# Kernel tuning notes

Hardware: AMD Instinct MI355X
Metric: run time of the kernel (lower is better)

The kernel has to match this reference:

```python
import jax, jax.numpy as jnp
import numpy as np

N = 100000
E = 1600000
IN_DIM, HID, OUT = 128, 64, 32
SLOPE = 0.1


def setup_inputs() -> dict:
    key = jax.random.key(0)
    ks = jax.random.split(key, 8)
    x = jax.random.normal(ks[0], (N, IN_DIM), dtype=jnp.float32)
    edge_index = jax.random.randint(ks[1], (2, E), 0, N, dtype=jnp.int64)
    s1 = 1.0 / np.sqrt(IN_DIM)
    s2 = 1.0 / np.sqrt(HID)
    W_l1 = jax.random.uniform(ks[2], (IN_DIM, HID), jnp.float32, -s1, s1)
    W_r1 = jax.random.uniform(ks[3], (IN_DIM, HID), jnp.float32, -s1, s1)
    b1 = jax.random.uniform(ks[4], (HID,), jnp.float32, -s1, s1)
    W_l2 = jax.random.uniform(ks[5], (HID, OUT), jnp.float32, -s2, s2)
    W_r2 = jax.random.uniform(ks[6], (HID, OUT), jnp.float32, -s2, s2)
    b2 = jax.random.uniform(ks[7], (OUT,), jnp.float32, -s2, s2)
    return {"x": x, "edge_index": edge_index,
            "W_l1": W_l1, "W_r1": W_r1, "b1": b1,
            "W_l2": W_l2, "W_r2": W_r2, "b2": b2}


def _sage_conv(h, src, dst, deg_inv, W_l, W_r, b):
    # mean-aggregate neighbor features: gather from src, scatter-add to dst
    agg = jax.ops.segment_sum(h[src], dst, num_segments=N) * deg_inv  # [N, d]
    return agg @ W_l + h @ W_r + b


def reference(x, edge_index, W_l1, W_r1, b1, W_l2, W_r2, b2):
    src, dst = edge_index[0], edge_index[1]
    deg = jax.ops.segment_sum(jnp.ones((E,), x.dtype), dst, num_segments=N)
    deg_inv = (1.0 / jnp.maximum(deg, 1.0))[:, None]  # [N, 1]
    h = jax.nn.leaky_relu(_sage_conv(x, src, dst, deg_inv, W_l1, W_r1, b1), SLOPE)
    z = jax.nn.leaky_relu(_sage_conv(h, src, dst, deg_inv, W_l2, W_r2, b2), SLOPE)
    return z
```

## Files before the change

### kernel.cpp

```cpp
#include <hip/hip_runtime.h>


constexpr int IN_DIM  = 128;
constexpr int HID     = 64;
constexpr int OUT_DIM = 32;
constexpr float SLOPE = 0.1f;
constexpr int NPB_SHIFT = 8;
constexpr int NBMAX = 512;
constexpr int CHUNK = 4096;

typedef unsigned int uint32;
typedef unsigned short ushort16;

__device__ inline float blo(uint32 u) { return __uint_as_float(u << 16); }
__device__ inline float bhi(uint32 u) { return __uint_as_float(u & 0xffff0000u); }
__device__ inline ushort16 f2b(float f) {
    uint32 u = __float_as_uint(f);
    u += 0x7fffu + ((u >> 16) & 1u);
    return (ushort16)(u >> 16);
}
__device__ inline uint32 pack2(float lo, float hi) {
    return (uint32)f2b(lo) | ((uint32)f2b(hi) << 16);
}

__global__ __launch_bounds__(256) void bucket_hist_kernel(
    const int* __restrict__ dst, int* __restrict__ bhist, int E) {
    __shared__ int bh[NBMAX];
    for (int i = threadIdx.x; i < NBMAX; i += 256) bh[i] = 0;
    __syncthreads();
    for (int e = blockIdx.x * 256 + threadIdx.x; e < E; e += gridDim.x * 256)
        atomicAdd(&bh[dst[e] >> NPB_SHIFT], 1);
    __syncthreads();
    for (int b = threadIdx.x; b < NBMAX; b += 256)
        if (bh[b]) atomicAdd(&bhist[b], bh[b]);
}

__global__ __launch_bounds__(512) void bucket_scan_kernel(
    const int* __restrict__ bhist, int* __restrict__ ebase,
    int* __restrict__ pbase, int* __restrict__ bcur,
    int* __restrict__ rowptr, int NB, int N, int E) {
    __shared__ int s1[512], s2[512];
    const int t = threadIdx.x;
    int bh = (t < NB) ? bhist[t] : 0;
    int pd = (bh + 15) & ~15;
    s1[t] = bh; s2[t] = pd; __syncthreads();
    for (int off = 1; off < 512; off <<= 1) {
        int a = (t >= off) ? s1[t - off] : 0;
        int b = (t >= off) ? s2[t - off] : 0;
        __syncthreads();
        s1[t] += a; s2[t] += b;
        __syncthreads();
    }
    ebase[t] = s1[t] - bh;
    pbase[t] = s2[t] - pd;
    bcur[t]  = s2[t] - pd;
    if (t == 0) rowptr[N] = E;
}

__global__ __launch_bounds__(256) void partition_kernel(
    const int* __restrict__ src, const int* __restrict__ dst,
    int* __restrict__ bcur, uint32* __restrict__ pairs, int E, int NB) {
    __shared__ int hist[NBMAX], loff[NBMAX], cur[NBMAX];
    __shared__ int s[256];
    __shared__ uint32 stage[CHUNK];
    const int tid = threadIdx.x;
    const int e0  = blockIdx.x * CHUNK;
    const int cnt = min(CHUNK, E - e0);
    for (int i = tid; i < NBMAX; i += 256) hist[i] = 0;
    __syncthreads();
    int sreg[16], dreg[16];
#pragma unroll
    for (int k = 0; k < 16; ++k) {
        int i = tid + k * 256;
        if (i < cnt) {
            sreg[k] = src[e0 + i];
            dreg[k] = dst[e0 + i];
            atomicAdd(&hist[dreg[k] >> NPB_SHIFT], 1);
        }
    }
    __syncthreads();
    int a0 = hist[2 * tid], a1 = hist[2 * tid + 1];
    s[tid] = a0 + a1; __syncthreads();
    for (int off = 1; off < 256; off <<= 1) {
        int t = (tid >= off) ? s[tid - off] : 0;
        __syncthreads();
        s[tid] += t;
        __syncthreads();
    }
    int ex = s[tid] - (a0 + a1);
    loff[2 * tid] = ex;      loff[2 * tid + 1] = ex + a0;
    cur[2 * tid]  = ex;      cur[2 * tid + 1]  = ex + a0;
    __syncthreads();
#pragma unroll
    for (int k = 0; k < 16; ++k) {
        int i = tid + k * 256;
        if (i < cnt) {
            int b = dreg[k] >> NPB_SHIFT;
            int pos = atomicAdd(&cur[b], 1);
            stage[pos] = (uint32)sreg[k] | ((uint32)(dreg[k] & 255) << 24);
        }
    }
    __syncthreads();
    for (int b = tid; b < NB; b += 256) {
        int cb = hist[b];
        if (cb) {
            int g  = atomicAdd(&bcur[b], cb);
            int lb = loff[b];
            for (int k = 0; k < cb; ++k) pairs[g + k] = stage[lb + k];
        }
    }
}

__global__ __launch_bounds__(256) void fine_bin_kernel(
    const uint32* __restrict__ pairs, const int* __restrict__ bhist,
    const int* __restrict__ ebase, const int* __restrict__ pbase,
    int* __restrict__ rowptr, int* __restrict__ srcs, int N) {
    __shared__ int h2[256], cur[256], s[256];
    const int tid  = threadIdx.x;
    const int b    = blockIdx.x;
    const int n0   = b << NPB_SHIFT;
    const int base = pbase[b];
    const int sz   = bhist[b];
    h2[tid] = 0;
    __syncthreads();
    for (int i = tid; i < sz; i += 256)
        atomicAdd(&h2[pairs[base + i] >> 24], 1);
    __syncthreads();
    int v = h2[tid]; s[tid] = v; __syncthreads();
    for (int off = 1; off < 256; off <<= 1) {
        int t = (tid >= off) ? s[tid - off] : 0;
        __syncthreads();
        s[tid] += t;
        __syncthreads();
    }
    int rp = ebase[b] + s[tid] - v;
    int n  = n0 + tid;
    if (n < N) rowptr[n] = rp;
    cur[tid] = rp;
    __syncthreads();
    for (int i = tid; i < sz; i += 256) {
        uint32 u = pairs[base + i];
        int p = atomicAdd(&cur[u >> 24], 1);
        srcs[p] = (int)(u & 0xFFFFFFu);
    }
}

__global__ __launch_bounds__(256) void gemm1_mfma_kernel(
    const float* __restrict__ x, const float* __restrict__ Wl,
    const float* __restrict__ Wr, const float* __restrict__ b1,
    ushort16* __restrict__ xl, float* __restrict__ xr, int N) {
    using frag = __attribute__((ext_vector_type(8))) short;
    using f32x4 = __attribute__((ext_vector_type(4))) float;
    constexpr int LDA = IN_DIM + 8;
    __shared__ ushort16 Ash[64][LDA];
    __shared__ ushort16 Bsh[128][LDA];
    const int tid = threadIdx.x;
    const int n0  = blockIdx.x * 64;
    {
        const int c = tid & 63;
        for (int k = tid >> 6; k < IN_DIM; k += 4) {
            Bsh[c][k]      = f2b(Wl[k * HID + c]);
            Bsh[c + 64][k] = f2b(Wr[k * HID + c]);
        }
    }
    {
        const int lc  = (tid & 31) * 4;
        for (int row = tid >> 5; row < 64; row += 8) {
            int node = n0 + row;
            float4 xv = (node < N)
                ? *reinterpret_cast<const float4*>(&x[(long)node * IN_DIM + lc])
                : float4{0.f, 0.f, 0.f, 0.f};
            ushort16 pk[4] = {f2b(xv.x), f2b(xv.y), f2b(xv.z), f2b(xv.w)};
            *reinterpret_cast<ushort2*>(&Ash[row][lc])     = ushort2{pk[0], pk[1]};
            *reinterpret_cast<ushort2*>(&Ash[row][lc + 2]) = ushort2{pk[2], pk[3]};
        }
    }
    __syncthreads();
    const int lane = tid & 63;
    const int m0   = (tid >> 6) * 16;
    const int mlo  = lane & 15;
    const int qk   = lane >> 4;
    frag Af[4];
#pragma unroll
    for (int kc = 0; kc < 4; ++kc)
        Af[kc] = *reinterpret_cast<const frag*>(&Ash[m0 + mlo][kc * 32 + qk * 8]);
#pragma unroll
    for (int ct = 0; ct < 8; ++ct) {
        f32x4 acc = {0.f, 0.f, 0.f, 0.f};
#pragma unroll
        for (int kc = 0; kc < 4; ++kc) {
            frag Bf = *reinterpret_cast<const frag*>(&Bsh[ct * 16 + mlo][kc * 32 + qk * 8]);
            acc = __builtin_amdgcn_mfma_f32_16x16x32_bf16(Af[kc], Bf, acc, 0, 0, 0);
        }
        const int col = ct * 16 + mlo;
#pragma unroll
        for (int r = 0; r < 4; ++r) {
            int node = n0 + m0 + qk * 4 + r;
            if (node < N) {
                if (col < HID) xl[(long)node * HID + col] = f2b(acc[r]);
                else           xr[(long)node * HID + (col - HID)] = acc[r] + b1[col - HID];
            }
        }
    }
}

__global__ __launch_bounds__(256) void agg_mid_kernel(
    const int* __restrict__ rowptr, const int* __restrict__ srcs,
    const uint4* __restrict__ xlq,
    const float* __restrict__ xr,
    const float* __restrict__ Wl2, const float* __restrict__ Wr2,
    const float* __restrict__ b2,
    uint4* __restrict__ hlq,
    float* __restrict__ hr, int N) {
    __shared__ float Wc[HID][HID];
    for (int i = threadIdx.x; i < HID * HID; i += 256) {
        int k = i >> 6, c = i & 63;
        Wc[k][c] = (c < OUT_DIM) ? Wl2[k * OUT_DIM + c]
                                 : Wr2[k * OUT_DIM + (c - OUT_DIM)];
    }
    __syncthreads();
    const int lane  = threadIdx.x & 63;
    const int li    = lane & 7;
    const int gbase = lane & 56;
    const int wave  = (blockIdx.x << 2) + (threadIdx.x >> 6);
    const int n     = wave * 8 + (lane >> 3);
    if (n >= N) return;
    const int rp = rowptr[n];
    const int d  = rowptr[n + 1] - rp;
    float acc[8] = {};
    int j = 0;
    while (j + 8 <= d) {
        int sidb = srcs[rp + j + li];
#pragma unroll
        for (int t = 0; t < 8; ++t) {
            int s = __shfl(sidb, gbase + t);
            uint4 u = xlq[(long)s * 8 + li];
            acc[0] += blo(u.x); acc[1] += bhi(u.x);
            acc[2] += blo(u.y); acc[3] += bhi(u.y);
            acc[4] += blo(u.z); acc[5] += bhi(u.z);
            acc[6] += blo(u.w); acc[7] += bhi(u.w);
        }
        j += 8;
    }
    int r = d - j;
    if (r > 0) {
        int sidb = srcs[rp + j + ((li < r) ? li : 0)];
#pragma unroll
        for (int t = 0; t < 7; ++t) {
            if (t < r) {
                int s = __shfl(sidb, gbase + t);
                uint4 u = xlq[(long)s * 8 + li];
                acc[0] += blo(u.x); acc[1] += bhi(u.x);
                acc[2] += blo(u.y); acc[3] += bhi(u.y);
                acc[4] += blo(u.z); acc[5] += bhi(u.z);
                acc[6] += blo(u.w); acc[7] += bhi(u.w);
            }
        }
    }
    const float dinv = (d > 0) ? (1.f / (float)d) : 1.f;
    float4 xrA = *reinterpret_cast<const float4*>(&xr[(long)n * HID + 8 * li]);
    float4 xrB = *reinterpret_cast<const float4*>(&xr[(long)n * HID + 8 * li + 4]);
    float h[8];
    h[0] = fmaf(acc[0], dinv, xrA.x); h[1] = fmaf(acc[1], dinv, xrA.y);
    h[2] = fmaf(acc[2], dinv, xrA.z); h[3] = fmaf(acc[3], dinv, xrA.w);
    h[4] = fmaf(acc[4], dinv, xrB.x); h[5] = fmaf(acc[5], dinv, xrB.y);
    h[6] = fmaf(acc[6], dinv, xrB.z); h[7] = fmaf(acc[7], dinv, xrB.w);
#pragma unroll
    for (int t = 0; t < 8; ++t) h[t] = (h[t] > 0.f) ? h[t] : SLOPE * h[t];
    float o[8] = {};
#pragma unroll
    for (int k = 0; k < HID; ++k) {
        float hk = __shfl(h[k & 7], gbase + (k >> 3));
        float4 wA = *reinterpret_cast<const float4*>(&Wc[k][8 * li]);
        float4 wB = *reinterpret_cast<const float4*>(&Wc[k][8 * li + 4]);
        o[0] = fmaf(hk, wA.x, o[0]); o[1] = fmaf(hk, wA.y, o[1]);
        o[2] = fmaf(hk, wA.z, o[2]); o[3] = fmaf(hk, wA.w, o[3]);
        o[4] = fmaf(hk, wB.x, o[4]); o[5] = fmaf(hk, wB.y, o[5]);
        o[6] = fmaf(hk, wB.z, o[6]); o[7] = fmaf(hk, wB.w, o[7]);
    }
    if (li < 4) {
        uint4 pk;
        pk.x = pack2(o[0], o[1]); pk.y = pack2(o[2], o[3]);
        pk.z = pack2(o[4], o[5]); pk.w = pack2(o[6], o[7]);
        hlq[(long)n * 4 + li] = pk;
    } else {
        int c0 = 8 * li - 32;
        float4 bA = *reinterpret_cast<const float4*>(&b2[c0]);
        float4 bB = *reinterpret_cast<const float4*>(&b2[c0 + 4]);
        float4 vA = {o[0] + bA.x, o[1] + bA.y, o[2] + bA.z, o[3] + bA.w};
        float4 vB = {o[4] + bB.x, o[5] + bB.y, o[6] + bB.z, o[7] + bB.w};
        *reinterpret_cast<float4*>(&hr[(long)n * OUT_DIM + c0]) = vA;
        *reinterpret_cast<float4*>(&hr[(long)n * OUT_DIM + c0 + 4]) = vB;
    }
}

__global__ __launch_bounds__(256) void agg2_final_kernel(
    const int* __restrict__ rowptr, const int* __restrict__ srcs,
    const uint4* __restrict__ hlq,
    const float* __restrict__ hr,
    float* __restrict__ z, int N) {
    const int lane  = threadIdx.x & 63;
    const int li    = lane & 3;
    const int gbase = lane & 60;
    const int wave  = (blockIdx.x << 2) + (threadIdx.x >> 6);
    const int n     = wave * 16 + (lane >> 2);
    if (n >= N) return;
    const int rp = rowptr[n];
    const int d  = rowptr[n + 1] - rp;
    float acc[8] = {};
    int j = 0;
    while (j + 8 <= d) {
        int sA = srcs[rp + j + li];
        int sB = srcs[rp + j + 4 + li];
#pragma unroll
        for (int t = 0; t < 4; ++t) {
            int s0 = __shfl(sA, gbase + t);
            int s1 = __shfl(sB, gbase + t);
            uint4 u0 = hlq[(long)s0 * 4 + li];
            uint4 u1 = hlq[(long)s1 * 4 + li];
            acc[0] += blo(u0.x); acc[1] += bhi(u0.x);
            acc[2] += blo(u0.y); acc[3] += bhi(u0.y);
            acc[4] += blo(u0.z); acc[5] += bhi(u0.z);
            acc[6] += blo(u0.w); acc[7] += bhi(u0.w);
            acc[0] += blo(u1.x); acc[1] += bhi(u1.x);
            acc[2] += blo(u1.y); acc[3] += bhi(u1.y);
            acc[4] += blo(u1.z); acc[5] += bhi(u1.z);
            acc[6] += blo(u1.w); acc[7] += bhi(u1.w);
        }
        j += 8;
    }
    int r = d - j;
    if (r > 0) {
        int sA = srcs[rp + j + ((li < r) ? li : 0)];
        int sB = srcs[rp + j + ((4 + li < r) ? 4 + li : 0)];
#pragma unroll
        for (int t = 0; t < 4; ++t) {
            if (t < r) {
                int s = __shfl(sA, gbase + t);
                uint4 u = hlq[(long)s * 4 + li];
                acc[0] += blo(u.x); acc[1] += bhi(u.x);
                acc[2] += blo(u.y); acc[3] += bhi(u.y);
                acc[4] += blo(u.z); acc[5] += bhi(u.z);
                acc[6] += blo(u.w); acc[7] += bhi(u.w);
            }
            if (t + 4 < r) {
                int s = __shfl(sB, gbase + t);
                uint4 u = hlq[(long)s * 4 + li];
                acc[0] += blo(u.x); acc[1] += bhi(u.x);
                acc[2] += blo(u.y); acc[3] += bhi(u.y);
                acc[4] += blo(u.z); acc[5] += bhi(u.z);
                acc[6] += blo(u.w); acc[7] += bhi(u.w);
            }
        }
    }
    const float dinv = (d > 0) ? (1.f / (float)d) : 1.f;
    float4 hA = *reinterpret_cast<const float4*>(&hr[(long)n * OUT_DIM + 8 * li]);
    float4 hB = *reinterpret_cast<const float4*>(&hr[(long)n * OUT_DIM + 8 * li + 4]);
    float4 vA, vB;
    vA.x = fmaf(acc[0], dinv, hA.x); vA.y = fmaf(acc[1], dinv, hA.y);
    vA.z = fmaf(acc[2], dinv, hA.z); vA.w = fmaf(acc[3], dinv, hA.w);
    vB.x = fmaf(acc[4], dinv, hB.x); vB.y = fmaf(acc[5], dinv, hB.y);
    vB.z = fmaf(acc[6], dinv, hB.z); vB.w = fmaf(acc[7], dinv, hB.w);
    vA.x = (vA.x > 0.f) ? vA.x : SLOPE * vA.x;
    vA.y = (vA.y > 0.f) ? vA.y : SLOPE * vA.y;
    vA.z = (vA.z > 0.f) ? vA.z : SLOPE * vA.z;
    vA.w = (vA.w > 0.f) ? vA.w : SLOPE * vA.w;
    vB.x = (vB.x > 0.f) ? vB.x : SLOPE * vB.x;
    vB.y = (vB.y > 0.f) ? vB.y : SLOPE * vB.y;
    vB.z = (vB.z > 0.f) ? vB.z : SLOPE * vB.z;
    vB.w = (vB.w > 0.f) ? vB.w : SLOPE * vB.w;
    *reinterpret_cast<float4*>(&z[(long)n * OUT_DIM + 8 * li]) = vA;
    *reinterpret_cast<float4*>(&z[(long)n * OUT_DIM + 8 * li + 4]) = vB;
}

extern "C" void kernel_launch(void* const* d_in, const int* in_sizes, int n_in,
                              void* d_out, int out_size, void* d_ws, size_t ws_size,
                              hipStream_t stream) {
    const float* x   = (const float*)d_in[0];
    const int*   ei  = (const int*)d_in[1];
    const float* Wl1 = (const float*)d_in[2];
    const float* Wr1 = (const float*)d_in[3];
    const float* b1  = (const float*)d_in[4];
    const float* Wl2 = (const float*)d_in[5];
    const float* Wr2 = (const float*)d_in[6];
    const float* b2  = (const float*)d_in[7];

    const int N = in_sizes[0] / IN_DIM;
    const int E = in_sizes[1] / 2;
    const int* src = ei;
    const int* dst = ei + E;
    const int NB = (N + 255) >> NPB_SHIFT;

    char* p = (char*)d_ws;
    int* bhist    = (int*)p;           p += sizeof(int) * NBMAX;
    int* ebase    = (int*)p;           p += sizeof(int) * NBMAX;
    int* pbase    = (int*)p;           p += sizeof(int) * NBMAX;
    int* bcur     = (int*)p;           p += sizeof(int) * NBMAX;
    int* rowptr   = (int*)p;           p += sizeof(int) * (N + 4);
    uint32* pairs = (uint32*)p;        p += sizeof(uint32) * ((size_t)E + 16 * NBMAX);
    int* srcs     = (int*)p;           p += sizeof(int) * E;
    ushort16* xl  = (ushort16*)p;      p += sizeof(ushort16) * (size_t)N * HID;
    float* xr     = (float*)p;         p += sizeof(float) * (size_t)N * HID;
    ushort16* hl  = (ushort16*)p;      p += sizeof(ushort16) * (size_t)N * OUT_DIM;
    float* hr     = (float*)p;         p += sizeof(float) * (size_t)N * OUT_DIM;

    hipMemsetAsync(bhist, 0, sizeof(int) * NBMAX, stream);

    bucket_hist_kernel<<<512, 256, 0, stream>>>(dst, bhist, E);
    bucket_scan_kernel<<<1, 512, 0, stream>>>(bhist, ebase, pbase, bcur, rowptr, NB, N, E);
    partition_kernel<<<(E + CHUNK - 1) / CHUNK, 256, 0, stream>>>(src, dst, bcur, pairs, E, NB);
    fine_bin_kernel<<<NB, 256, 0, stream>>>(pairs, bhist, ebase, pbase, rowptr, srcs, N);
    gemm1_mfma_kernel<<<(N + 63) / 64, 256, 0, stream>>>(x, Wl1, Wr1, b1, xl, xr, N);
    agg_mid_kernel<<<(N + 31) / 32, 256, 0, stream>>>(rowptr, srcs, (const uint4*)xl, xr,
                                                      Wl2, Wr2, b2, (uint4*)hl, hr, N);
    agg2_final_kernel<<<(N + 63) / 64, 256, 0, stream>>>(rowptr, srcs, (const uint4*)hl, hr,
                                                         (float*)d_out, N);
}
```

Before: 279.0 us.

## Split layer-2 GEMM into MFMA kernel and batch gather loads in aggregation kernels

The fused aggregation+FMA-GEMM kernel is split into an aggregation kernel that writes h as bf16 and a separate MFMA bf16 GEMM kernel for the layer-2 weights. Both aggregation loops now issue 16 independent gather loads before accumulating, to raise memory-level parallelism. This adds an extra N×64 bf16 round trip and a kernel launch, uses bf16 weights for layer 2, and raises register pressure from the batched loads.

```diff
diff --git a/kernel.cpp b/kernel.cpp
--- a/kernel.cpp
+++ b/kernel.cpp
@@ -21,6 +21,12 @@
 }
 __device__ inline uint32 pack2(float lo, float hi) {
     return (uint32)f2b(lo) | ((uint32)f2b(hi) << 16);
+}
+__device__ inline void addup(float* acc, uint4 u) {
+    acc[0] += blo(u.x); acc[1] += bhi(u.x);
+    acc[2] += blo(u.y); acc[3] += bhi(u.y);
+    acc[4] += blo(u.z); acc[5] += bhi(u.z);
+    acc[6] += blo(u.w); acc[7] += bhi(u.w);
 }
 
 __global__ __launch_bounds__(256) void bucket_hist_kernel(
@@ -204,21 +210,11 @@
     }
 }
 
-__global__ __launch_bounds__(256) void agg_mid_kernel(
+__global__ __launch_bounds__(256) void agg1_kernel(
     const int* __restrict__ rowptr, const int* __restrict__ srcs,
     const uint4* __restrict__ xlq,
     const float* __restrict__ xr,
-    const float* __restrict__ Wl2, const float* __restrict__ Wr2,
-    const float* __restrict__ b2,
-    uint4* __restrict__ hlq,
-    float* __restrict__ hr, int N) {
-    __shared__ float Wc[HID][HID];
-    for (int i = threadIdx.x; i < HID * HID; i += 256) {
-        int k = i >> 6, c = i & 63;
-        Wc[k][c] = (c < OUT_DIM) ? Wl2[k * OUT_DIM + c]
-                                 : Wr2[k * OUT_DIM + (c - OUT_DIM)];
-    }
-    __syncthreads();
+    uint4* __restrict__ hq, int N) {
     const int lane  = threadIdx.x & 63;
     const int li    = lane & 7;
     const int gbase = lane & 56;
@@ -229,31 +225,45 @@
     const int d  = rowptr[n + 1] - rp;
     float acc[8] = {};
     int j = 0;
-    while (j + 8 <= d) {
-        int sidb = srcs[rp + j + li];
+    while (j + 16 <= d) {
+        int sA = srcs[rp + j + li];
+        int sB = srcs[rp + j + 8 + li];
+        uint4 u0[8], u1[8];
 #pragma unroll
         for (int t = 0; t < 8; ++t) {
-            int s = __shfl(sidb, gbase + t);
-            uint4 u = xlq[(long)s * 8 + li];
-            acc[0] += blo(u.x); acc[1] += bhi(u.x);
-            acc[2] += blo(u.y); acc[3] += bhi(u.y);
-            acc[4] += blo(u.z); acc[5] += bhi(u.z);
-            acc[6] += blo(u.w); acc[7] += bhi(u.w);
-        }
+            int s = __shfl(sA, gbase + t);
+            u0[t] = xlq[(long)s * 8 + li];
+        }
+#pragma unroll
+        for (int t = 0; t < 8; ++t) {
+            int s = __shfl(sB, gbase + t);
+            u1[t] = xlq[(long)s * 8 + li];
+        }
+#pragma unroll
+        for (int t = 0; t < 8; ++t) { addup(acc, u0[t]); addup(acc, u1[t]); }
+        j += 16;
+    }
+    if (j + 8 <= d) {
+        int sA = srcs[rp + j + li];
+        uint4 u0[8];
+#pragma unroll
+        for (int t = 0; t < 8; ++t) {
+            int s = __shfl(sA, gbase + t);
+            u0[t] = xlq[(long)s * 8 + li];
+        }
+#pragma unroll
+        for (int t = 0; t < 8; ++t) addup(acc, u0[t]);
         j += 8;
     }
     int r = d - j;
     if (r > 0) {
-        int sidb = srcs[rp + j + ((li < r) ? li : 0)];
+        int sA = srcs[rp + j + ((li < r) ? li : 0)];
 #pragma unroll
         for (int t = 0; t < 7; ++t) {
             if (t < r) {
-                int s = __shfl(sidb, gbase + t);
+                int s = __shfl(sA, gbase + t);
                 uint4 u = xlq[(long)s * 8 + li];
-                acc[0] += blo(u.x); acc[1] += bhi(u.x);
-                acc[2] += blo(u.y); acc[3] += bhi(u.y);
-                acc[4] += blo(u.z); acc[5] += bhi(u.z);
-                acc[6] += blo(u.w); acc[7] += bhi(u.w);
+                addup(acc, u);
             }
         }
     }
@@ -267,30 +277,57 @@
     h[6] = fmaf(acc[6], dinv, xrB.z); h[7] = fmaf(acc[7], dinv, xrB.w);
 #pragma unroll
     for (int t = 0; t < 8; ++t) h[t] = (h[t] > 0.f) ? h[t] : SLOPE * h[t];
-    float o[8] = {};
-#pragma unroll
-    for (int k = 0; k < HID; ++k) {
-        float hk = __shfl(h[k & 7], gbase + (k >> 3));
-        float4 wA = *reinterpret_cast<const float4*>(&Wc[k][8 * li]);
-        float4 wB = *reinterpret_cast<const float4*>(&Wc[k][8 * li + 4]);
-        o[0] = fmaf(hk, wA.x, o[0]); o[1] = fmaf(hk, wA.y, o[1]);
-        o[2] = fmaf(hk, wA.z, o[2]); o[3] = fmaf(hk, wA.w, o[3]);
-        o[4] = fmaf(hk, wB.x, o[4]); o[5] = fmaf(hk, wB.y, o[5]);
-        o[6] = fmaf(hk, wB.z, o[6]); o[7] = fmaf(hk, wB.w, o[7]);
-    }
-    if (li < 4) {
-        uint4 pk;
-        pk.x = pack2(o[0], o[1]); pk.y = pack2(o[2], o[3]);
-        pk.z = pack2(o[4], o[5]); pk.w = pack2(o[6], o[7]);
-        hlq[(long)n * 4 + li] = pk;
-    } else {
-        int c0 = 8 * li - 32;
-        float4 bA = *reinterpret_cast<const float4*>(&b2[c0]);
-        float4 bB = *reinterpret_cast<const float4*>(&b2[c0 + 4]);
-        float4 vA = {o[0] + bA.x, o[1] + bA.y, o[2] + bA.z, o[3] + bA.w};
-        float4 vB = {o[4] + bB.x, o[5] + bB.y, o[6] + bB.z, o[7] + bB.w};
-        *reinterpret_cast<float4*>(&hr[(long)n * OUT_DIM + c0]) = vA;
-        *reinterpret_cast<float4*>(&hr[(long)n * OUT_DIM + c0 + 4]) = vB;
+    uint4 pk;
+    pk.x = pack2(h[0], h[1]); pk.y = pack2(h[2], h[3]);
+    pk.z = pack2(h[4], h[5]); pk.w = pack2(h[6], h[7]);
+    hq[(long)n * 8 + li] = pk;
+}
+
+__global__ __launch_bounds__(256) void gemm2_mfma_kernel(
+    const ushort16* __restrict__ hs, const float* __restrict__ Wl2,
+    const float* __restrict__ Wr2, const float* __restrict__ b2,
+    ushort16* __restrict__ hl, float* __restrict__ hr, int N) {
+    using frag = __attribute__((ext_vector_type(8))) short;
+    using f32x4 = __attribute__((ext_vector_type(4))) float;
+    __shared__ ushort16 Bsh[64][72];
+    const int tid = threadIdx.x;
+    const int n0  = blockIdx.x * 64;
+    {
+        const int c = tid & 63;
+        for (int k = tid >> 6; k < HID; k += 4) {
+            float w = (c < OUT_DIM) ? Wl2[k * OUT_DIM + c]
+                                    : Wr2[k * OUT_DIM + (c - OUT_DIM)];
+            Bsh[c][k] = f2b(w);
+        }
+    }
+    __syncthreads();
+    const int lane = tid & 63;
+    const int m0   = (tid >> 6) * 16;
+    const int mlo  = lane & 15;
+    const int qk   = lane >> 4;
+    const int row  = n0 + m0 + mlo;
+    const int arow = (row < N) ? row : 0;
+    frag Af[2];
+#pragma unroll
+    for (int kc = 0; kc < 2; ++kc)
+        Af[kc] = *reinterpret_cast<const frag*>(&hs[(long)arow * HID + kc * 32 + qk * 8]);
+#pragma unroll
+    for (int ct = 0; ct < 4; ++ct) {
+        f32x4 acc = {0.f, 0.f, 0.f, 0.f};
+#pragma unroll
+        for (int kc = 0; kc < 2; ++kc) {
+            frag Bf = *reinterpret_cast<const frag*>(&Bsh[ct * 16 + mlo][kc * 32 + qk * 8]);
+            acc = __builtin_amdgcn_mfma_f32_16x16x32_bf16(Af[kc], Bf, acc, 0, 0, 0);
+        }
+        const int col = ct * 16 + mlo;
+#pragma unroll
+        for (int r = 0; r < 4; ++r) {
+            int node = n0 + m0 + qk * 4 + r;
+            if (node < N) {
+                if (col < OUT_DIM) hl[(long)node * OUT_DIM + col] = f2b(acc[r]);
+                else hr[(long)node * OUT_DIM + (col - OUT_DIM)] = acc[r] + b2[col - OUT_DIM];
+            }
+        }
     }
 }
 
@@ -309,47 +346,41 @@
     const int d  = rowptr[n + 1] - rp;
     float acc[8] = {};
     int j = 0;
-    while (j + 8 <= d) {
+    while (j + 16 <= d) {
         int sA = srcs[rp + j + li];
         int sB = srcs[rp + j + 4 + li];
-#pragma unroll
-        for (int t = 0; t < 4; ++t) {
-            int s0 = __shfl(sA, gbase + t);
-            int s1 = __shfl(sB, gbase + t);
-            uint4 u0 = hlq[(long)s0 * 4 + li];
-            uint4 u1 = hlq[(long)s1 * 4 + li];
-            acc[0] += blo(u0.x); acc[1] += bhi(u0.x);
-            acc[2] += blo(u0.y); acc[3] += bhi(u0.y);
-            acc[4] += blo(u0.z); acc[5] += bhi(u0.z);
-            acc[6] += blo(u0.w); acc[7] += bhi(u0.w);
-            acc[0] += blo(u1.x); acc[1] += bhi(u1.x);
-            acc[2] += blo(u1.y); acc[3] += bhi(u1.y);
-            acc[4] += blo(u1.z); acc[5] += bhi(u1.z);
-            acc[6] += blo(u1.w); acc[7] += bhi(u1.w);
-        }
-        j += 8;
+        int sC = srcs[rp + j + 8 + li];
+        int sD = srcs[rp + j + 12 + li];
+        uint4 u[16];
+#pragma unroll
+        for (int t = 0; t < 4; ++t) u[t]      = hlq[(long)__shfl(sA, gbase + t) * 4 + li];
+#pragma unroll
+        for (int t = 0; t < 4; ++t) u[4 + t]  = hlq[(long)__shfl(sB, gbase + t) * 4 + li];
+#pragma unroll
+        for (int t = 0; t < 4; ++t) u[8 + t]  = hlq[(long)__shfl(sC, gbase + t) * 4 + li];
+#pragma unroll
+        for (int t = 0; t < 4; ++t) u[12 + t] = hlq[(long)__shfl(sD, gbase + t) * 4 + li];
+#pragma unroll
+        for (int t = 0; t < 16; ++t) addup(acc, u[t]);
+        j += 16;
+    }
+    while (j + 4 <= d) {
+        int sA = srcs[rp + j + li];
+        uint4 u[4];
+#pragma unroll
+        for (int t = 0; t < 4; ++t) u[t] = hlq[(long)__shfl(sA, gbase + t) * 4 + li];
+#pragma unroll
+        for (int t = 0; t < 4; ++t) addup(acc, u[t]);
+        j += 4;
     }
     int r = d - j;
     if (r > 0) {
         int sA = srcs[rp + j + ((li < r) ? li : 0)];
-        int sB = srcs[rp + j + ((4 + li < r) ? 4 + li : 0)];
-#pragma unroll
-        for (int t = 0; t < 4; ++t) {
+#pragma unroll
+        for (int t = 0; t < 3; ++t) {
             if (t < r) {
-                int s = __shfl(sA, gbase + t);
-                uint4 u = hlq[(long)s * 4 + li];
-                acc[0] += blo(u.x); acc[1] += bhi(u.x);
-                acc[2] += blo(u.y); acc[3] += bhi(u.y);
-                acc[4] += blo(u.z); acc[5] += bhi(u.z);
-                acc[6] += blo(u.w); acc[7] += bhi(u.w);
-            }
-            if (t + 4 < r) {
-                int s = __shfl(sB, gbase + t);
-                uint4 u = hlq[(long)s * 4 + li];
-                acc[0] += blo(u.x); acc[1] += bhi(u.x);
-                acc[2] += blo(u.y); acc[3] += bhi(u.y);
-                acc[4] += blo(u.z); acc[5] += bhi(u.z);
-                acc[6] += blo(u.w); acc[7] += bhi(u.w);
+                uint4 u = hlq[(long)__shfl(sA, gbase + t) * 4 + li];
+                addup(acc, u);
             }
         }
     }
@@ -401,6 +432,7 @@
     int* srcs     = (int*)p;           p += sizeof(int) * E;
     ushort16* xl  = (ushort16*)p;      p += sizeof(ushort16) * (size_t)N * HID;
     float* xr     = (float*)p;         p += sizeof(float) * (size_t)N * HID;
+    ushort16* h   = (ushort16*)p;      p += sizeof(ushort16) * (size_t)N * HID;
     ushort16* hl  = (ushort16*)p;      p += sizeof(ushort16) * (size_t)N * OUT_DIM;
     float* hr     = (float*)p;         p += sizeof(float) * (size_t)N * OUT_DIM;
 
@@ -411,8 +443,9 @@
     partition_kernel<<<(E + CHUNK - 1) / CHUNK, 256, 0, stream>>>(src, dst, bcur, pairs, E, NB);
     fine_bin_kernel<<<NB, 256, 0, stream>>>(pairs, bhist, ebase, pbase, rowptr, srcs, N);
     gemm1_mfma_kernel<<<(N + 63) / 64, 256, 0, stream>>>(x, Wl1, Wr1, b1, xl, xr, N);
-    agg_mid_kernel<<<(N + 31) / 32, 256, 0, stream>>>(rowptr, srcs, (const uint4*)xl, xr,
-                                                      Wl2, Wr2, b2, (uint4*)hl, hr, N);
+    agg1_kernel<<<(N + 31) / 32, 256, 0, stream>>>(rowptr, srcs, (const uint4*)xl, xr,
+                                                   (uint4*)h, N);
+    gemm2_mfma_kernel<<<(N + 63) / 64, 256, 0, stream>>>(h, Wl2, Wr2, b2, hl, hr, N);
     agg2_final_kernel<<<(N + 63) / 64, 256, 0, stream>>>(rowptr, srcs, (const uint4*)hl, hr,
                                                          (float*)d_out, N);
 }
```

After: 279.1 us. About the same (+0.0%).
